# Optimization experiments

Measured on AMD Instinct MI355X. Metric: run time of the kernel, lower is better.

## Reference

```python
import jax, jax.numpy as jnp
import numpy as np

B, L, H = 2, 1024, 1024   # batch, seq_len, hidden_size
NH, D, K = 16, 64, 4      # num_heads, head_dim, conv kernel
HD = NH * D


def setup_inputs() -> dict:
    key = jax.random.key(0)
    ks = jax.random.split(key, 12)
    s = 0.02  # LeCun-ish init scale as in the torch module
    return {
        "hidden_states": jax.random.normal(ks[0], (B, L, H), jnp.float32),
        "Wq": jax.random.normal(ks[1], (HD, H), jnp.float32) * s,
        "bq": jnp.zeros((HD,), jnp.float32),
        "Wk": jax.random.normal(ks[2], (HD, H), jnp.float32) * s,
        "bk": jnp.zeros((HD,), jnp.float32),
        "Wv": jax.random.normal(ks[3], (HD, H), jnp.float32) * s,
        "bv": jnp.zeros((HD,), jnp.float32),
        "Wa": jax.random.normal(ks[4], (NH, H), jnp.float32) * s,
        "Wb": jax.random.normal(ks[5], (NH, H), jnp.float32) * s,
        "Wconv": jax.random.normal(ks[6], (HD, 1, K), jnp.float32) * s,
        "Wo": jax.random.normal(ks[7], (H, HD), jnp.float32) * s,
        "bo": jnp.zeros((H,), jnp.float32),
    }


def _gated_delta(q, k, v, alpha, beta):
    # q,k,v: [B,L,NH,D]; alpha,beta: [B,L,NH]
    # S_t = S_{t-1} @ (alpha_t * (I - beta_t k_t k_t^T)) + beta_t v_t k_t^T ; o_t = S_t q_t
    eye = jnp.eye(q.shape[-1], dtype=q.dtype)

    def step(S, xs):
        q_t, k_t, v_t, a_t, b_t = xs  # [B,NH,D], [B,NH]
        kk = jnp.einsum('bhd,bhe->bhde', k_t, k_t)
        decay = a_t[..., None, None] * (eye - b_t[..., None, None] * kk)
        S = jnp.einsum('bhde,bhef->bhdf', S, decay) \
            + b_t[..., None, None] * jnp.einsum('bhd,bhe->bhde', v_t, k_t)
        o_t = jnp.einsum('bhde,bhe->bhd', S, q_t)
        return S, o_t

    xs = (jnp.moveaxis(q, 1, 0), jnp.moveaxis(k, 1, 0), jnp.moveaxis(v, 1, 0),
          jnp.moveaxis(alpha, 1, 0), jnp.moveaxis(beta, 1, 0))
    S0 = jnp.zeros((q.shape[0], q.shape[2], q.shape[3], q.shape[3]), q.dtype)
    _, outs = jax.lax.scan(step, S0, xs)  # [L,B,NH,D]
    return jnp.transpose(outs, (1, 2, 0, 3))  # [B,NH,L,D] (matches torch stack+transposes)


def reference(hidden_states, Wq, bq, Wk, bk, Wv, bv, Wa, Wb, Wconv, Wo, bo):
    Bc, Lc, Hc = hidden_states.shape
    q = (hidden_states @ Wq.T + bq).reshape(Bc, Lc, NH, D)
    k = (hidden_states @ Wk.T + bk).reshape(Bc, Lc, NH, D)
    v = (hidden_states @ Wv.T + bv).reshape(Bc, Lc, NH, D)
    alpha = jax.nn.sigmoid(hidden_states @ Wa.T)   # [B,L,NH]
    beta = jax.nn.softplus(hidden_states @ Wb.T)   # [B,L,NH]

    out = _gated_delta(q, k, v, alpha, beta)       # [B,NH,L,D]
    out = out.reshape(Bc, Lc, NH * D)              # replicates torch's reshape of [B,NH,L,D]
    x = jnp.transpose(out, (0, 2, 1))              # [B,HD,L]
    conv = jax.lax.conv_general_dilated(
        x, Wconv, window_strides=(1,), padding=[(K - 1, 0)],
        feature_group_count=NH * D, dimension_numbers=('NCH', 'OIH', 'NCH'))
    x = x + conv                                   # residual depthwise causal conv
    x = jnp.transpose(x, (0, 2, 1))                # [B,L,HD]
    return x @ Wo.T + bo                           # [B,L,H]; dropout is identity at eval
```

## Files before the change

### kernel.cpp

```cpp
#include <hip/hip_runtime.h>
#include <math.h>

#define BB 2
#define LL 1024
#define HH 1024
#define NH 16
#define DD 64
#define HD (NH * DD)
#define MM (BB * LL)
#define RCT 32
#define KEXT 3072
#define NBK 1088

typedef _Float16 f16x8 __attribute__((ext_vector_type(8)));
typedef _Float16 f16x4 __attribute__((ext_vector_type(4)));
typedef float f32x4 __attribute__((ext_vector_type(4)));

__device__ __forceinline__ void load_lds16(const void* g, void* l) {
    __builtin_amdgcn_global_load_lds(
        (const __attribute__((address_space(1))) void*)g,
        (__attribute__((address_space(3))) void*)l, 16, 0, 0);
}

__global__ __launch_bounds__(256) void convert_front(
    const float* __restrict__ hs,
    const float* __restrict__ Wq, const float* __restrict__ Wk,
    const float* __restrict__ Wv, const float* __restrict__ Wa,
    const float* __restrict__ Wb, const float* __restrict__ Wo,
    _Float16* __restrict__ Ae3,
    _Float16* __restrict__ Bk, _Float16* __restrict__ Bqv,
    _Float16* __restrict__ Be2)
{
    const int blk = blockIdx.x;
    const int t = threadIdx.x;

    if (blk < 2048) {
        float4 x = *(const float4*)(hs + (size_t)blk * 1024 + t * 4);
        x.x *= 16.f; x.y *= 16.f; x.z *= 16.f; x.w *= 16.f;
        f16x4 h, l;
        h[0] = (_Float16)x.x; l[0] = (_Float16)(x.x - (float)h[0]);
        h[1] = (_Float16)x.y; l[1] = (_Float16)(x.y - (float)h[1]);
        h[2] = (_Float16)x.z; l[2] = (_Float16)(x.z - (float)h[2]);
        h[3] = (_Float16)x.w; l[3] = (_Float16)(x.w - (float)h[3]);
        _Float16* base = Ae3 + (size_t)blk * KEXT + t * 4;
        *(f16x4*)(base)        = h;
        *(f16x4*)(base + 1024) = l;
        *(f16x4*)(base + 2048) = h;
        return;
    }
    if (blk < 3136) {
        const int n = blk - 2048;
        const float* src = nullptr;
        if (n < 1024)      src = Wk + (size_t)n * 1024;
        else if (n < 1040) src = Wa + (size_t)(n - 1024) * 1024;
        else if (n < 1056) src = Wb + (size_t)(n - 1040) * 1024;
        float4 x = src ? *(const float4*)(src + t * 4)
                       : make_float4(0.f, 0.f, 0.f, 0.f);
        x.x *= 64.f; x.y *= 64.f; x.z *= 64.f; x.w *= 64.f;
        f16x4 h, l;
        h[0] = (_Float16)x.x; l[0] = (_Float16)(x.x - (float)h[0]);
        h[1] = (_Float16)x.y; l[1] = (_Float16)(x.y - (float)h[1]);
        h[2] = (_Float16)x.z; l[2] = (_Float16)(x.z - (float)h[2]);
        h[3] = (_Float16)x.w; l[3] = (_Float16)(x.w - (float)h[3]);
        _Float16* base = Bk + (size_t)n * KEXT + t * 4;
        *(f16x4*)(base)        = h;
        *(f16x4*)(base + 1024) = h;
        *(f16x4*)(base + 2048) = l;
        return;
    }
    if (blk < 5184) {
        const int n = blk - 3136;
        const float* src = (n < 1024) ? Wq + (size_t)n * 1024
                                      : Wv + (size_t)(n - 1024) * 1024;
        float4 x = *(const float4*)(src + t * 4);
        f16x4 h;
        h[0] = (_Float16)(x.x * 64.f);
        h[1] = (_Float16)(x.y * 64.f);
        h[2] = (_Float16)(x.z * 64.f);
        h[3] = (_Float16)(x.w * 64.f);
        *(f16x4*)(Bqv + (size_t)n * 1024 + t * 4) = h;
        return;
    }
    {
        const int n = blk - 5184;
        float4 x = *(const float4*)(Wo + (size_t)n * 1024 + t * 4);
        f16x4 h;
        h[0] = (_Float16)(x.x * 64.f);
        h[1] = (_Float16)(x.y * 64.f);
        h[2] = (_Float16)(x.z * 64.f);
        h[3] = (_Float16)(x.w * 64.f);
        *(f16x4*)(Be2 + (size_t)n * 1024 + t * 4) = h;
    }
}

__global__ __launch_bounds__(256) void mfma_gemm_proj(
    const _Float16* __restrict__ Ae3, const _Float16* __restrict__ Bk,
    const _Float16* __restrict__ Bqv,
    float* __restrict__ qkv, float* __restrict__ ab,
    const float* __restrict__ bq, const float* __restrict__ bk,
    const float* __restrict__ bv)
{
    __shared__ __align__(16) _Float16 As[2][128 * 32];
    __shared__ __align__(16) _Float16 Bs[2][128 * 32];

    const int blk = blockIdx.x;
    const int tid = threadIdx.x;
    const int wave = tid >> 6;
    const int lane = tid & 63;
    const int srow = lane >> 2;
    const int scol = (lane & 3) * 8;
    const int fm = lane & 15;
    const int fq = (lane >> 4) * 8;
    const int rquad = (lane >> 4) * 4;

    if (blk < 272) {
        const int bm = (blk / 17) * 128;
        const int bn = (blk % 17) * 64;
        const int wr = (wave >> 1) * 64;
        const int wc = (wave & 1) * 32;

        const _Float16* gA0 = Ae3 + (size_t)(bm + wave * 32 + srow) * KEXT + scol;
        const _Float16* gA1 = gA0 + (size_t)16 * KEXT;
        const _Float16* gB0 = Bk + (size_t)(bn + wave * 16 + srow) * KEXT + scol;
        _Float16* lA0_0 = &As[0][(wave * 32) * 32];
        _Float16* lA1_0 = &As[0][(wave * 32 + 16) * 32];
        _Float16* lB0_0 = &Bs[0][(wave * 16) * 32];
        _Float16* lA0_1 = &As[1][(wave * 32) * 32];
        _Float16* lA1_1 = &As[1][(wave * 32 + 16) * 32];
        _Float16* lB0_1 = &Bs[1][(wave * 16) * 32];

        f32x4 acc[4][2] = {};

        for (int k0 = 0; k0 < KEXT; k0 += 64) {
            load_lds16(gA0 + k0,      lA0_0);
            load_lds16(gA1 + k0,      lA1_0);
            load_lds16(gB0 + k0,      lB0_0);
            load_lds16(gA0 + k0 + 32, lA0_1);
            load_lds16(gA1 + k0 + 32, lA1_1);
            load_lds16(gB0 + k0 + 32, lB0_1);
            __syncthreads();

            #pragma unroll
            for (int s = 0; s < 2; ++s) {
                f16x8 a[4], b[2];
                #pragma unroll
                for (int mt = 0; mt < 4; ++mt)
                    a[mt] = *(const f16x8*)&As[s][(wr + mt * 16 + fm) * 32 + fq];
                #pragma unroll
                for (int nt = 0; nt < 2; ++nt)
                    b[nt] = *(const f16x8*)&Bs[s][(wc + nt * 16 + fm) * 32 + fq];
                #pragma unroll
                for (int mt = 0; mt < 4; ++mt)
                    #pragma unroll
                    for (int nt = 0; nt < 2; ++nt)
                        acc[mt][nt] = __builtin_amdgcn_mfma_f32_16x16x32_f16(
                            a[mt], b[nt], acc[mt][nt], 0, 0, 0);
            }
            __syncthreads();
        }

        #pragma unroll
        for (int mt = 0; mt < 4; ++mt) {
            #pragma unroll
            for (int nt = 0; nt < 2; ++nt) {
                const int col = bn + wc + nt * 16 + fm;
                #pragma unroll
                for (int i = 0; i < 4; ++i) {
                    const int row = bm + wr + mt * 16 + rquad + i;
                    float val = acc[mt][nt][i] * (1.0f / 1024.0f);
                    if (col < 1024)
                        qkv[(size_t)row * 3072 + 1024 + col] = val + bk[col];
                    else if (col < 1040)
                        ab[(size_t)row * 32 + (col - 1024)] =
                            1.f / (1.f + expf(-val));
                    else if (col < 1056)
                        ab[(size_t)row * 32 + 16 + (col - 1040)] =
                            fmaxf(val, 0.f) + log1pf(expf(-fabsf(val)));
                }
            }
        }
    } else {
        const int n = blk - 272;
        const int bm = (n / 16) * 128;
        const int bn = (n % 16) * 128;
        const int wr = (wave >> 1) * 64;
        const int wc = (wave & 1) * 64;

        const _Float16* gA0 = Ae3 + (size_t)(bm + wave * 32 + srow) * KEXT + scol;
        const _Float16* gA1 = gA0 + (size_t)16 * KEXT;
        const _Float16* gB0 = Bqv + (size_t)(bn + wave * 32 + srow) * 1024 + scol;
        const _Float16* gB1 = gB0 + (size_t)16 * 1024;
        _Float16* lA0_0 = &As[0][(wave * 32) * 32];
        _Float16* lA1_0 = &As[0][(wave * 32 + 16) * 32];
        _Float16* lB0_0 = &Bs[0][(wave * 32) * 32];
        _Float16* lB1_0 = &Bs[0][(wave * 32 + 16) * 32];
        _Float16* lA0_1 = &As[1][(wave * 32) * 32];
        _Float16* lA1_1 = &As[1][(wave * 32 + 16) * 32];
        _Float16* lB0_1 = &Bs[1][(wave * 32) * 32];
        _Float16* lB1_1 = &Bs[1][(wave * 32 + 16) * 32];

        f32x4 acc[4][4] = {};

        for (int k0 = 0; k0 < 1024; k0 += 64) {
            load_lds16(gA0 + k0,      lA0_0);
            load_lds16(gA1 + k0,      lA1_0);
            load_lds16(gB0 + k0,      lB0_0);
            load_lds16(gB1 + k0,      lB1_0);
            load_lds16(gA0 + k0 + 32, lA0_1);
            load_lds16(gA1 + k0 + 32, lA1_1);
            load_lds16(gB0 + k0 + 32, lB0_1);
            load_lds16(gB1 + k0 + 32, lB1_1);
            __syncthreads();

            #pragma unroll
            for (int s = 0; s < 2; ++s) {
                f16x8 a[4], b[4];
                #pragma unroll
                for (int mt = 0; mt < 4; ++mt)
                    a[mt] = *(const f16x8*)&As[s][(wr + mt * 16 + fm) * 32 + fq];
                #pragma unroll
                for (int nt = 0; nt < 4; ++nt)
                    b[nt] = *(const f16x8*)&Bs[s][(wc + nt * 16 + fm) * 32 + fq];
                #pragma unroll
                for (int mt = 0; mt < 4; ++mt)
                    #pragma unroll
                    for (int nt = 0; nt < 4; ++nt)
                        acc[mt][nt] = __builtin_amdgcn_mfma_f32_16x16x32_f16(
                            a[mt], b[nt], acc[mt][nt], 0, 0, 0);
            }
            __syncthreads();
        }

        #pragma unroll
        for (int mt = 0; mt < 4; ++mt) {
            #pragma unroll
            for (int nt = 0; nt < 4; ++nt) {
                const int col = bn + wc + nt * 16 + fm;
                #pragma unroll
                for (int i = 0; i < 4; ++i) {
                    const int row = bm + wr + mt * 16 + rquad + i;
                    float val = acc[mt][nt][i] * (1.0f / 1024.0f);
                    if (col < 1024)
                        qkv[(size_t)row * 3072 + col] = val + bq[col];
                    else
                        qkv[(size_t)row * 3072 + 1024 + col] = val + bv[col - 1024];
                }
            }
        }
    }
}

__global__ __launch_bounds__(256) void mfma_gemm_out(
    const _Float16* __restrict__ Ae2, const _Float16* __restrict__ Be2,
    float* __restrict__ outp, const float* __restrict__ bo)
{
    __shared__ __align__(16) _Float16 As[2][128 * 32];
    __shared__ __align__(16) _Float16 Bs[2][64 * 32];

    const int tid = threadIdx.x;
    const int wave = tid >> 6;
    const int lane = tid & 63;
    const int bm = blockIdx.y * 128;
    const int bn = blockIdx.x * 64;
    const int wr = (wave >> 1) * 64;
    const int wc = (wave & 1) * 32;

    const int srow = lane >> 2;
    const int scol = (lane & 3) * 8;
    const _Float16* gA0 = Ae2 + (size_t)(bm + wave * 32 + srow) * 1024 + scol;
    const _Float16* gA1 = gA0 + (size_t)16 * 1024;
    const _Float16* gB0 = Be2 + (size_t)(bn + wave * 16 + srow) * 1024 + scol;
    _Float16* lA0_0 = &As[0][(wave * 32) * 32];
    _Float16* lA1_0 = &As[0][(wave * 32 + 16) * 32];
    _Float16* lB0_0 = &Bs[0][(wave * 16) * 32];
    _Float16* lA0_1 = &As[1][(wave * 32) * 32];
    _Float16* lA1_1 = &As[1][(wave * 32 + 16) * 32];
    _Float16* lB0_1 = &Bs[1][(wave * 16) * 32];

    const int fm = lane & 15;
    const int fq = (lane >> 4) * 8;

    f32x4 acc[4][2] = {};

    for (int k0 = 0; k0 < 1024; k0 += 64) {
        load_lds16(gA0 + k0,      lA0_0);
        load_lds16(gA1 + k0,      lA1_0);
        load_lds16(gB0 + k0,      lB0_0);
        load_lds16(gA0 + k0 + 32, lA0_1);
        load_lds16(gA1 + k0 + 32, lA1_1);
        load_lds16(gB0 + k0 + 32, lB0_1);
        __syncthreads();

        #pragma unroll
        for (int s = 0; s < 2; ++s) {
            f16x8 a[4], b[2];
            #pragma unroll
            for (int mt = 0; mt < 4; ++mt)
                a[mt] = *(const f16x8*)&As[s][(wr + mt * 16 + fm) * 32 + fq];
            #pragma unroll
            for (int nt = 0; nt < 2; ++nt)
                b[nt] = *(const f16x8*)&Bs[s][(wc + nt * 16 + fm) * 32 + fq];
            #pragma unroll
            for (int mt = 0; mt < 4; ++mt)
                #pragma unroll
                for (int nt = 0; nt < 2; ++nt)
                    acc[mt][nt] = __builtin_amdgcn_mfma_f32_16x16x32_f16(
                        a[mt], b[nt], acc[mt][nt], 0, 0, 0);
        }
        __syncthreads();
    }

    const int rquad = (lane >> 4) * 4;
    #pragma unroll
    for (int mt = 0; mt < 4; ++mt) {
        #pragma unroll
        for (int nt = 0; nt < 2; ++nt) {
            const int col = bn + wc + nt * 16 + fm;
            #pragma unroll
            for (int i = 0; i < 4; ++i) {
                const int row = bm + wr + mt * 16 + rquad + i;
                outp[(size_t)row * 1024 + col] = acc[mt][nt][i] * 64.f + bo[col];
            }
        }
    }
}

template <int CTRL>
__device__ __forceinline__ float dpp_addf(float x) {
    int y = __builtin_amdgcn_update_dpp(0, __builtin_bit_cast(int, x),
                                        CTRL, 0xF, 0xF, true);
    return x + __builtin_bit_cast(float, y);
}
__device__ __forceinline__ float red16(float x) {
    x = dpp_addf<0xB1>(x);
    x = dpp_addf<0x4E>(x);
    x = dpp_addf<0x124>(x);
    x = dpp_addf<0x128>(x);
    return x;
}

__global__ __launch_bounds__(64) void gdn_recurrence(
    const float* __restrict__ qkv, const float* __restrict__ ab,
    float* __restrict__ att)
{
    __shared__ __align__(16) float ks[2][RCT][64];
    __shared__ __align__(16) float qs[2][RCT][64];
    __shared__ __align__(16) float vs_[2][RCT][4];
    __shared__ __align__(16) float gab[2][RCT][2];

    const int blk = blockIdx.x;
    const int bh = blk & 31;
    const int s  = blk >> 5;
    const int b  = bh >> 4;
    const int h  = bh & 15;
    const int lane = threadIdx.x;
    const int rl = lane >> 4;
    const int el = lane & 15;
    const int e0 = el * 4;
    const int r0 = s * 4;

    const float* qb  = qkv + (size_t)b * LL * 3072 + h * 64;
    const float* kb  = qb + 1024;
    const float* vb  = qb + 2048 + r0;
    const float* abp = ab + (size_t)b * LL * 32 + h;
    float* op = att + ((size_t)(b * NH + h) * DD + r0 + rl) * LL;

    const int st = lane >> 4;
    const int sd = (lane & 15) * 4;

    float S0 = 0.f, S1 = 0.f, S2 = 0.f, S3 = 0.f;

    {
        const size_t ro = (size_t)st * 3072 + sd;
        #pragma unroll
        for (int m = 0; m < 8; ++m) {
            load_lds16(kb + ro + (size_t)m * 4 * 3072, &ks[0][m * 4][0]);
            load_lds16(qb + ro + (size_t)m * 4 * 3072, &qs[0][m * 4][0]);
        }
        float4 pv = make_float4(0.f,0.f,0.f,0.f);
        if (lane < RCT) pv = *(const float4*)(vb + (size_t)lane * 3072);
        float pab = (lane < 32) ? abp[(size_t)lane * 32]
                                : abp[(size_t)(lane - 32) * 32 + 16];
        if (lane < RCT) *(float4*)&vs_[0][lane][0] = pv;
        if (lane < 32) gab[0][lane][0] = pab;
        else           gab[0][lane - 32][1] = pab;
    }
    __syncthreads();

    const int NCHUNK = LL / RCT;
    for (int c = 0; c < NCHUNK; ++c) {
        const int cur = c & 1, nxt = cur ^ 1;
        const bool more = (c + 1 < NCHUNK);

        float4 pv = make_float4(0.f,0.f,0.f,0.f);
        float pab = 0.f;
        if (more) {
            const size_t t0 = (size_t)(c + 1) * RCT;
            const size_t ro = (t0 + st) * 3072 + sd;
            #pragma unroll
            for (int m = 0; m < 8; ++m) {
                load_lds16(kb + ro + (size_t)m * 4 * 3072, &ks[nxt][m * 4][0]);
                load_lds16(qb + ro + (size_t)m * 4 * 3072, &qs[nxt][m * 4][0]);
            }
            if (lane < RCT) pv = *(const float4*)(vb + (t0 + lane) * 3072);
            pab = (lane < 32) ? abp[(t0 + lane) * 32]
                              : abp[(t0 + lane - 32) * 32 + 16];
        }

        float4 kr[8], qr[8];
        float vr[8];
        float2 abr[8];
        #pragma unroll
        for (int i = 0; i < 6; ++i) {
            kr[i] = *(const float4*)&ks[cur][i][e0];
            qr[i] = *(const float4*)&qs[cur][i][e0];
            vr[i] = vs_[cur][i][rl];
            abr[i] = *(const float2*)&gab[cur][i][0];
        }

        float o0 = 0.f, o1 = 0.f, o2 = 0.f;
        #pragma unroll 8
        for (int t = 0; t < RCT; ++t) {
            const int tf = (t + 6 < RCT) ? t + 6 : RCT - 1;
            kr[(t + 6) & 7] = *(const float4*)&ks[cur][tf][e0];
            qr[(t + 6) & 7] = *(const float4*)&qs[cur][tf][e0];
            vr[(t + 6) & 7] = vs_[cur][tf][rl];
            abr[(t + 6) & 7] = *(const float2*)&gab[cur][tf][0];

            const float4 kc = kr[t & 7];
            const float4 qc = qr[t & 7];
            const float vc = vr[t & 7];
            const float ac = abr[t & 7].x;
            const float bc = abr[t & 7].y;

            float p0 = fmaf(S1, kc.y, S0 * kc.x);
            float p1 = fmaf(S3, kc.w, S2 * kc.z);
            float sk = red16(p0 + p1);

            const float cf = bc * fmaf(-ac, sk, vc);

            S0 = fmaf(ac, S0, cf * kc.x);
            S1 = fmaf(ac, S1, cf * kc.y);
            S2 = fmaf(ac, S2, cf * kc.z);
            S3 = fmaf(ac, S3, cf * kc.w);

            float q0 = fmaf(S1, qc.y, S0 * qc.x);
            float q1 = fmaf(S3, qc.w, S2 * qc.z);
            float o = red16(q0 + q1);

            const int ph = t & 3;
            if (ph == 0) o0 = o;
            else if (ph == 1) o1 = o;
            else if (ph == 2) o2 = o;
            else if (el == 0)
                *(float4*)(op + c * RCT + t - 3) = make_float4(o0, o1, o2, o);
        }

        if (more) {
            if (lane < RCT) *(float4*)&vs_[nxt][lane][0] = pv;
            if (lane < 32) gab[nxt][lane][0] = pab;
            else           gab[nxt][lane - 32][1] = pab;
        }
        __syncthreads();
    }
}

__global__ __launch_bounds__(256) void conv_convert(
    const float* __restrict__ att, const float* __restrict__ Wconv,
    _Float16* __restrict__ Ae2)
{
    __shared__ float yt[112][68];
    const int lb = blockIdx.x;
    const int h  = blockIdx.y;
    const int b  = blockIdx.z;
    const int tid = threadIdx.x;

    {
        const int d = tid >> 2;
        const int part = tid & 3;
        const float* src  = att + ((size_t)(b * NH + h) * DD + d) * LL;
        const float* srcm = src - (size_t)DD * LL;
        #pragma unroll
        for (int m = 0; m < 7; ++m) {
            const int off = (part * 7 + m) * 4;
            const int lg = lb * 64 - 48 + off;
            float4 v;
            if (lg >= 0)      v = *(const float4*)(src + lg);
            else if (h > 0)   v = *(const float4*)(srcm + lg + 1024);
            else              v = make_float4(0.f, 0.f, 0.f, 0.f);
            yt[off + 0][d] = v.x; yt[off + 1][d] = v.y;
            yt[off + 2][d] = v.z; yt[off + 3][d] = v.w;
        }
    }
    __syncthreads();

    float4 w[4];
    #pragma unroll
    for (int k = 0; k < 4; ++k)
        w[k] = ((const float4*)Wconv)[tid * 4 + k];

    const int d0 = (tid & 15) * 4;
    const int lq = tid >> 4;
    const float sc = 1.f / 4096.f;

    #pragma unroll
    for (int rr = 0; rr < 4; ++rr) {
        const int ll = rr * 16 + lq;
        float y0[4], y1[4], y2[4], y3[4];
        *(float4*)y0 = *(const float4*)&yt[ll +  0][d0];
        *(float4*)y1 = *(const float4*)&yt[ll + 16][d0];
        *(float4*)y2 = *(const float4*)&yt[ll + 32][d0];
        *(float4*)y3 = *(const float4*)&yt[ll + 48][d0];
        f16x4 hi;
        #pragma unroll
        for (int k = 0; k < 4; ++k) {
            float acc = y3[k];
            acc = fmaf(w[k].x, y0[k], acc);
            acc = fmaf(w[k].y, y1[k], acc);
            acc = fmaf(w[k].z, y2[k], acc);
            acc = fmaf(w[k].w, y3[k], acc);
            hi[k] = (_Float16)(acc * sc);
        }
        const size_t row = (size_t)b * 1024 + h * 64 + lb * 4 + rr;
        *(f16x4*)(Ae2 + row * 1024 + tid * 4) = hi;
    }
}

extern "C" void kernel_launch(void* const* d_in, const int* in_sizes, int n_in,
                              void* d_out, int out_size, void* d_ws, size_t ws_size,
                              hipStream_t stream)
{
    const float* hs    = (const float*)d_in[0];
    const float* Wq    = (const float*)d_in[1];
    const float* bq    = (const float*)d_in[2];
    const float* Wk    = (const float*)d_in[3];
    const float* bk    = (const float*)d_in[4];
    const float* Wv    = (const float*)d_in[5];
    const float* bv    = (const float*)d_in[6];
    const float* Wa    = (const float*)d_in[7];
    const float* Wb    = (const float*)d_in[8];
    const float* Wconv = (const float*)d_in[9];
    const float* Wo    = (const float*)d_in[10];
    const float* bo    = (const float*)d_in[11];
    float* out = (float*)d_out;

    char* w = (char*)d_ws;
    float* qkv = (float*)w;        w += (size_t)MM * 3072 * 4;
    float* att = (float*)w;        w += (size_t)MM * 1024 * 4;
    float* ab  = (float*)w;        w += (size_t)MM * 32 * 4;
    _Float16* Ae3 = (_Float16*)w;  w += (size_t)MM * KEXT * 2;
    _Float16* Bk  = (_Float16*)w;  w += (size_t)NBK * KEXT * 2;
    _Float16* Bqv = (_Float16*)w;  w += (size_t)2048 * 1024 * 2;
    _Float16* Ae2 = (_Float16*)w;  w += (size_t)MM * 1024 * 2;
    _Float16* Be2 = (_Float16*)w;  w += (size_t)1024 * 1024 * 2;

    hipLaunchKernelGGL(convert_front, dim3(6208), dim3(256), 0, stream,
                       hs, Wq, Wk, Wv, Wa, Wb, Wo, Ae3, Bk, Bqv, Be2);

    hipLaunchKernelGGL(mfma_gemm_proj, dim3(528), dim3(256), 0, stream,
                       Ae3, Bk, Bqv, qkv, ab, bq, bk, bv);

    hipLaunchKernelGGL(gdn_recurrence, dim3(512), dim3(64), 0, stream, qkv, ab, att);

    hipLaunchKernelGGL(conv_convert, dim3(16, 16, BB), dim3(256), 0, stream,
                       att, Wconv, Ae2);

    hipLaunchKernelGGL(mfma_gemm_out, dim3(1024 / 64, MM / 128), dim3(256), 0, stream,
                       Ae2, Be2, out, bo);
}
```

Measured before the change: 292.7 us.

## Batch LDS reads of recurrence operands into half-chunk register blocks

The gated-delta recurrence kernel now loads 16 timesteps of k, q, v, alpha and beta from LDS with explicit ds_read_b128 instructions before each half-chunk. It then waits once and runs the 16 steps fully unrolled from registers, replacing the rolling six-step prefetch. The v and alpha/beta shared buffers are transposed so each lane can fetch four timesteps with one vector read. This removes per-step LDS latency from the serial dependency chain, at the cost of many more live registers and inline asm that bypasses compiler scheduling.

Result: no change. 294.5 us (+0.6%).

```diff
diff --git a/kernel.cpp b/kernel.cpp
--- a/kernel.cpp
+++ b/kernel.cpp
@@ -339,14 +339,73 @@
     return x;
 }
 
+typedef __attribute__((address_space(3))) const float* lds_cfp;
+
+__device__ __forceinline__ float4 ds_read_f4(lds_cfp p) {
+    float4 d;
+    asm volatile("ds_read_b128 %0, %1" : "=v"(d) : "v"(p));
+    return d;
+}
+
+template <int I> struct RdKQ {
+    static __device__ __forceinline__ void go(float4* k, float4* q,
+                                              lds_cfp kb, lds_cfp qb) {
+        k[I] = ds_read_f4(kb + I * 64);
+        q[I] = ds_read_f4(qb + I * 64);
+        RdKQ<I + 1>::go(k, q, kb, qb);
+    }
+};
+template <> struct RdKQ<16> {
+    static __device__ __forceinline__ void go(float4*, float4*, lds_cfp, lds_cfp) {}
+};
+
+template <int I> struct RdVAB {
+    static __device__ __forceinline__ void go(float4* v, float4* a, float4* b,
+                                              lds_cfp vb, lds_cfp abb) {
+        v[I] = ds_read_f4(vb + I * 4);
+        a[I] = ds_read_f4(abb + I * 4);
+        b[I] = ds_read_f4(abb + RCT + I * 4);
+        RdVAB<I + 1>::go(v, a, b, vb, abb);
+    }
+};
+template <> struct RdVAB<4> {
+    static __device__ __forceinline__ void go(float4*, float4*, float4*, lds_cfp, lds_cfp) {}
+};
+
+#define GDN_STEP(T, TBASE)                                              \
+    {                                                                   \
+        const float4 kc = kv[T];                                        \
+        const float4 qc = qv[T];                                        \
+        const float vc = vv[(T) >> 2][(T) & 3];                         \
+        const float ac = av[(T) >> 2][(T) & 3];                         \
+        const float bc = bv[(T) >> 2][(T) & 3];                         \
+        float p0 = fmaf(S1, kc.y, S0 * kc.x);                           \
+        float p1 = fmaf(S3, kc.w, S2 * kc.z);                           \
+        float sk = red16(p0 + p1);                                      \
+        const float cf = bc * fmaf(-ac, sk, vc);                        \
+        S0 = fmaf(ac, S0, cf * kc.x);                                   \
+        S1 = fmaf(ac, S1, cf * kc.y);                                   \
+        S2 = fmaf(ac, S2, cf * kc.z);                                   \
+        S3 = fmaf(ac, S3, cf * kc.w);                                   \
+        float q0 = fmaf(S1, qc.y, S0 * qc.x);                           \
+        float q1 = fmaf(S3, qc.w, S2 * qc.z);                           \
+        float o = red16(q0 + q1);                                       \
+        const int ph = (T) & 3;                                         \
+        if (ph == 0) o0 = o;                                            \
+        else if (ph == 1) o1 = o;                                       \
+        else if (ph == 2) o2 = o;                                       \
+        else if (el == 0)                                               \
+            *(float4*)(op + (TBASE) + (T) - 3) = make_float4(o0, o1, o2, o); \
+    }
+
 __global__ __launch_bounds__(64) void gdn_recurrence(
     const float* __restrict__ qkv, const float* __restrict__ ab,
     float* __restrict__ att)
 {
     __shared__ __align__(16) float ks[2][RCT][64];
     __shared__ __align__(16) float qs[2][RCT][64];
-    __shared__ __align__(16) float vs_[2][RCT][4];
-    __shared__ __align__(16) float gab[2][RCT][2];
+    __shared__ __align__(16) float vs_t[2][4][RCT];
+    __shared__ __align__(16) float gab_t[2][2][RCT];
 
     const int blk = blockIdx.x;
     const int bh = blk & 31;
@@ -381,9 +440,14 @@
         if (lane < RCT) pv = *(const float4*)(vb + (size_t)lane * 3072);
         float pab = (lane < 32) ? abp[(size_t)lane * 32]
                                 : abp[(size_t)(lane - 32) * 32 + 16];
-        if (lane < RCT) *(float4*)&vs_[0][lane][0] = pv;
-        if (lane < 32) gab[0][lane][0] = pab;
-        else           gab[0][lane - 32][1] = pab;
+        if (lane < RCT) {
+            vs_t[0][0][lane] = pv.x;
+            vs_t[0][1][lane] = pv.y;
+            vs_t[0][2][lane] = pv.z;
+            vs_t[0][3][lane] = pv.w;
+        }
+        if (lane < 32) gab_t[0][0][lane] = pab;
+        else           gab_t[0][1][lane - 32] = pab;
     }
     __syncthreads();
 
@@ -407,59 +471,34 @@
                               : abp[(t0 + lane - 32) * 32 + 16];
         }
 
-        float4 kr[8], qr[8];
-        float vr[8];
-        float2 abr[8];
-        #pragma unroll
-        for (int i = 0; i < 6; ++i) {
-            kr[i] = *(const float4*)&ks[cur][i][e0];
-            qr[i] = *(const float4*)&qs[cur][i][e0];
-            vr[i] = vs_[cur][i][rl];
-            abr[i] = *(const float2*)&gab[cur][i][0];
-        }
-
+        float4 kv[16], qv[16], vv[4], av[4], bv[4];
         float o0 = 0.f, o1 = 0.f, o2 = 0.f;
-        #pragma unroll 8
-        for (int t = 0; t < RCT; ++t) {
-            const int tf = (t + 6 < RCT) ? t + 6 : RCT - 1;
-            kr[(t + 6) & 7] = *(const float4*)&ks[cur][tf][e0];
-            qr[(t + 6) & 7] = *(const float4*)&qs[cur][tf][e0];
-            vr[(t + 6) & 7] = vs_[cur][tf][rl];
-            abr[(t + 6) & 7] = *(const float2*)&gab[cur][tf][0];
-
-            const float4 kc = kr[t & 7];
-            const float4 qc = qr[t & 7];
-            const float vc = vr[t & 7];
-            const float ac = abr[t & 7].x;
-            const float bc = abr[t & 7].y;
-
-            float p0 = fmaf(S1, kc.y, S0 * kc.x);
-            float p1 = fmaf(S3, kc.w, S2 * kc.z);
-            float sk = red16(p0 + p1);
-
-            const float cf = bc * fmaf(-ac, sk, vc);
-
-            S0 = fmaf(ac, S0, cf * kc.x);
-            S1 = fmaf(ac, S1, cf * kc.y);
-            S2 = fmaf(ac, S2, cf * kc.z);
-            S3 = fmaf(ac, S3, cf * kc.w);
-
-            float q0 = fmaf(S1, qc.y, S0 * qc.x);
-            float q1 = fmaf(S3, qc.w, S2 * qc.z);
-            float o = red16(q0 + q1);
-
-            const int ph = t & 3;
-            if (ph == 0) o0 = o;
-            else if (ph == 1) o1 = o;
-            else if (ph == 2) o2 = o;
-            else if (el == 0)
-                *(float4*)(op + c * RCT + t - 3) = make_float4(o0, o1, o2, o);
-        }
+
+        RdKQ<0>::go(kv, qv, (lds_cfp)&ks[cur][0][e0], (lds_cfp)&qs[cur][0][e0]);
+        RdVAB<0>::go(vv, av, bv, (lds_cfp)&vs_t[cur][rl][0],
+                     (lds_cfp)&gab_t[cur][0][0]);
+        asm volatile("s_waitcnt lgkmcnt(0)" ::: "memory");
+        __builtin_amdgcn_sched_barrier(0);
+        #pragma unroll
+        for (int t = 0; t < 16; ++t) GDN_STEP(t, c * RCT);
+
+        RdKQ<0>::go(kv, qv, (lds_cfp)&ks[cur][16][e0], (lds_cfp)&qs[cur][16][e0]);
+        RdVAB<0>::go(vv, av, bv, (lds_cfp)&vs_t[cur][rl][16],
+                     (lds_cfp)&gab_t[cur][0][16]);
+        asm volatile("s_waitcnt lgkmcnt(0)" ::: "memory");
+        __builtin_amdgcn_sched_barrier(0);
+        #pragma unroll
+        for (int t = 0; t < 16; ++t) GDN_STEP(t, c * RCT + 16);
 
         if (more) {
-            if (lane < RCT) *(float4*)&vs_[nxt][lane][0] = pv;
-            if (lane < 32) gab[nxt][lane][0] = pab;
-            else           gab[nxt][lane - 32][1] = pab;
+            if (lane < RCT) {
+                vs_t[nxt][0][lane] = pv.x;
+                vs_t[nxt][1][lane] = pv.y;
+                vs_t[nxt][2][lane] = pv.z;
+                vs_t[nxt][3][lane] = pv.w;
+            }
+            if (lane < 32) gab_t[nxt][0][lane] = pab;
+            else           gab_t[nxt][1][lane - 32] = pab;
         }
         __syncthreads();
     }
```
